# Kernel optimization log

Measured on AMD Instinct MI355X. Metric: run time of the kernel, lower is better.

Reference implementation:

```python
import jax, jax.numpy as jnp
import numpy as np

N = 100000
IN_DIM = 512
OUT_DIM = 512


def setup_inputs() -> dict:
    key = jax.random.key(0)
    k1, k2, k3, k4 = jax.random.split(key, 4)
    x = jax.random.normal(k1, (N, IN_DIM), dtype=jnp.float32)
    edge_index = jax.random.randint(k2, (2, N), 0, N, dtype=jnp.int64)
    # Linear params (torch nn.Linear: out = x @ W.T + b)
    bound = 1.0 / np.sqrt(IN_DIM)
    W = jax.random.uniform(k3, (OUT_DIM, IN_DIM), minval=-bound, maxval=bound, dtype=jnp.float32)
    b = jax.random.uniform(k4, (OUT_DIM,), minval=-bound, maxval=bound, dtype=jnp.float32)
    return {"x": x, "edge_index": edge_index, "W": W, "b": b}


def reference(x, edge_index, W, b):
    # out = relu(linear(x))
    out = jax.nn.relu(jnp.einsum('ni,oi->no', x, W) + b)  # [N, OUT_DIM]
    # torch.scatter_add(out, 0, col[:, None], x):
    # index has shape [E, 1] so only column 0 of src (= x) is scattered:
    # out[col[e], 0] += x[e, 0]
    col = edge_index[1].astype(jnp.int32)  # [E], E == N here
    E = col.shape[0]
    out = out.at[col, 0].add(x[:E, 0])
    return out
```

## Files before the change

kernel.cpp:

```cpp
#include <hip/hip_runtime.h>
#include <stdint.h>

#define K_DIM 512
#define N_OUT 512
#define BM 128
#define BN 128
#define BK 64

typedef __bf16 bf16x8 __attribute__((ext_vector_type(8)));
typedef float f32x4 __attribute__((ext_vector_type(4)));
typedef unsigned short ushort8 __attribute__((ext_vector_type(8)));

__device__ inline unsigned short f2bf(float f) {
  unsigned u = __float_as_uint(f);
  u += 0x7fffu + ((u >> 16) & 1u);
  return (unsigned short)(u >> 16);
}

__global__ __launch_bounds__(256) void cvt_bf16_kernel(const float* __restrict__ src,
                                                       unsigned short* __restrict__ dst,
                                                       int n8) {
  int i = blockIdx.x * 256 + threadIdx.x;
  if (i >= n8) return;
  const float4* s = (const float4*)src + (size_t)i * 2;
  float4 a = s[0], c = s[1];
  ushort8 o;
  o[0] = f2bf(a.x); o[1] = f2bf(a.y); o[2] = f2bf(a.z); o[3] = f2bf(a.w);
  o[4] = f2bf(c.x); o[5] = f2bf(c.y); o[6] = f2bf(c.z); o[7] = f2bf(c.w);
  *(ushort8*)(dst + (size_t)i * 8) = o;
}

__global__ __launch_bounds__(256) void zero_f32_kernel(float* __restrict__ p, int n) {
  int i = blockIdx.x * 256 + threadIdx.x;
  if (i < n) p[i] = 0.f;
}

__global__ __launch_bounds__(256) void scatter_s_kernel(const float* __restrict__ x,
                                                        const int* __restrict__ ei,
                                                        float* __restrict__ s, int E) {
  int e = blockIdx.x * 256 + threadIdx.x;
  if (e < E) {
    int c = ei[E + e];
    atomicAdd(s + c, x[(size_t)e * K_DIM]);
  }
}

__global__ __launch_bounds__(256) void gemm_fused2_kernel(
    const float* __restrict__ x, const unsigned short* __restrict__ wb,
    const float* __restrict__ b, const float* __restrict__ s,
    float* __restrict__ out, int M) {
  __shared__ __align__(16) unsigned short Als[BM * BK];
  __shared__ __align__(16) unsigned short Bls[BN * BK];

  const int tid = threadIdx.x;
  const int lane = tid & 63;
  const int quad = lane >> 4;
  const int l16 = lane & 15;
  const int waveId = tid >> 6;
  const int wm = (waveId >> 1) * 64;
  const int wn = (waveId & 1) * 64;

  const int nwg = gridDim.x * gridDim.y;
  int raw = blockIdx.y * gridDim.x + blockIdx.x;
  int q = nwg >> 3, r = nwg & 7;
  int xcd = raw & 7;
  int wg = (xcd < r ? xcd * (q + 1) : r * (q + 1) + (xcd - r) * q) + (raw >> 3);
  const int blockM = (wg >> 2) * BM;
  const int blockN = (wg & 3) * BN;

  size_t goffA[4], goffB[4];
  int ldsoff[4];
#pragma unroll
  for (int i = 0; i < 4; ++i) {
    int ch = i * 256 + tid;
    int row = ch >> 3;
    int c8 = ch & 7;
    int sc = c8 ^ (row & 7);
    int ga_row = blockM + row;
    if (ga_row > M - 1) ga_row = M - 1;
    goffA[i] = (size_t)ga_row * K_DIM + sc * 8;
    goffB[i] = (size_t)(blockN + row) * K_DIM + sc * 8;
    ldsoff[i] = ch * 8;
  }

  f32x4 acc[4][4] = {};

  for (int k0 = 0; k0 < K_DIM; k0 += BK) {
    float4 a0[4], a1[4];
#pragma unroll
    for (int i = 0; i < 4; ++i) {
      a0[i] = *(const float4*)(x + goffA[i] + k0);
      a1[i] = *(const float4*)(x + goffA[i] + k0 + 4);
    }
#pragma unroll
    for (int i = 0; i < 4; ++i) {
      __builtin_amdgcn_global_load_lds(
          (const __attribute__((address_space(1))) void*)(wb + goffB[i] + k0),
          (__attribute__((address_space(3))) void*)(&Bls[ldsoff[i]]), 16, 0, 0);
    }
#pragma unroll
    for (int i = 0; i < 4; ++i) {
      ushort8 o;
      o[0] = f2bf(a0[i].x); o[1] = f2bf(a0[i].y); o[2] = f2bf(a0[i].z); o[3] = f2bf(a0[i].w);
      o[4] = f2bf(a1[i].x); o[5] = f2bf(a1[i].y); o[6] = f2bf(a1[i].z); o[7] = f2bf(a1[i].w);
      *(ushort8*)(&Als[ldsoff[i]]) = o;
    }
    __syncthreads();

#pragma unroll
    for (int ss = 0; ss < 2; ++ss) {
      bf16x8 af[4], bfr[4];
#pragma unroll
      for (int mi = 0; mi < 4; ++mi) {
        int rr = wm + mi * 16 + l16;
        int c = (ss * 4 + quad) ^ (rr & 7);
        af[mi] = *(const bf16x8*)(&Als[rr * BK + c * 8]);
      }
#pragma unroll
      for (int ni = 0; ni < 4; ++ni) {
        int rr = wn + ni * 16 + l16;
        int c = (ss * 4 + quad) ^ (rr & 7);
        bfr[ni] = *(const bf16x8*)(&Bls[rr * BK + c * 8]);
      }
#pragma unroll
      for (int mi = 0; mi < 4; ++mi)
#pragma unroll
        for (int ni = 0; ni < 4; ++ni)
          acc[mi][ni] = __builtin_amdgcn_mfma_f32_16x16x32_bf16(af[mi], bfr[ni], acc[mi][ni], 0, 0, 0);
    }
    __syncthreads();
  }

#pragma unroll
  for (int ni = 0; ni < 4; ++ni) {
    int gcol = blockN + wn + ni * 16 + l16;
    float bias = b[gcol];
#pragma unroll
    for (int mi = 0; mi < 4; ++mi) {
#pragma unroll
      for (int rr = 0; rr < 4; ++rr) {
        int grow = blockM + wm + mi * 16 + quad * 4 + rr;
        if (grow < M) {
          float v = acc[mi][ni][rr] + bias;
          v = v > 0.f ? v : 0.f;
          if (gcol == 0) v += s[grow];
          __builtin_nontemporal_store(v, out + (size_t)grow * N_OUT + gcol);
        }
      }
    }
  }
}

#define LDS_STRIDE 40
__global__ __launch_bounds__(256) void gemm_fused_kernel(
    const float* __restrict__ x, const float* __restrict__ W,
    const float* __restrict__ b, float* __restrict__ out, int M) {
  __shared__ __align__(16) unsigned short Als[BM * LDS_STRIDE];
  __shared__ __align__(16) unsigned short Bls[BN * LDS_STRIDE];
  const int tid = threadIdx.x;
  const int lane = tid & 63;
  const int quad = lane >> 4;
  const int l16 = lane & 15;
  const int waveId = tid >> 6;
  const int wm = (waveId >> 1) * 64;
  const int wn = (waveId & 1) * 64;
  const int blockM = blockIdx.y * BM;
  const int blockN = blockIdx.x * BN;
  f32x4 acc[4][4] = {};
  for (int k0 = 0; k0 < K_DIM; k0 += 32) {
#pragma unroll
    for (int i = 0; i < 4; ++i) {
      int idx = i * 256 + tid;
      int row = idx >> 3;
      int c4 = idx & 7;
      float4 va = make_float4(0.f, 0.f, 0.f, 0.f);
      int grow = blockM + row;
      if (grow < M) va = *(const float4*)(x + (size_t)grow * K_DIM + k0 + c4 * 4);
      ushort4 ha;
      ha.x = f2bf(va.x); ha.y = f2bf(va.y); ha.z = f2bf(va.z); ha.w = f2bf(va.w);
      *(ushort4*)(&Als[row * LDS_STRIDE + c4 * 4]) = ha;
      float4 vb = *(const float4*)(W + (size_t)(blockN + row) * K_DIM + k0 + c4 * 4);
      ushort4 hb;
      hb.x = f2bf(vb.x); hb.y = f2bf(vb.y); hb.z = f2bf(vb.z); hb.w = f2bf(vb.w);
      *(ushort4*)(&Bls[row * LDS_STRIDE + c4 * 4]) = hb;
    }
    __syncthreads();
    bf16x8 af[4], bfr[4];
#pragma unroll
    for (int mi = 0; mi < 4; ++mi)
      af[mi] = *(const bf16x8*)(&Als[(wm + mi * 16 + l16) * LDS_STRIDE + quad * 8]);
#pragma unroll
    for (int ni = 0; ni < 4; ++ni)
      bfr[ni] = *(const bf16x8*)(&Bls[(wn + ni * 16 + l16) * LDS_STRIDE + quad * 8]);
#pragma unroll
    for (int mi = 0; mi < 4; ++mi)
#pragma unroll
      for (int ni = 0; ni < 4; ++ni)
        acc[mi][ni] = __builtin_amdgcn_mfma_f32_16x16x32_bf16(af[mi], bfr[ni], acc[mi][ni], 0, 0, 0);
    __syncthreads();
  }
#pragma unroll
  for (int ni = 0; ni < 4; ++ni) {
    int gcol = blockN + wn + ni * 16 + l16;
    float bias = b[gcol];
#pragma unroll
    for (int mi = 0; mi < 4; ++mi) {
#pragma unroll
      for (int rr = 0; rr < 4; ++rr) {
        int grow = blockM + wm + mi * 16 + quad * 4 + rr;
        if (grow < M) {
          float v = acc[mi][ni][rr] + bias;
          out[(size_t)grow * N_OUT + gcol] = v > 0.f ? v : 0.f;
        }
      }
    }
  }
}

__global__ void scatter_kernel(const float* __restrict__ x,
                               const int* __restrict__ ei,
                               float* __restrict__ out, int E) {
  int e = blockIdx.x * 256 + threadIdx.x;
  if (e < E) {
    int c = ei[E + e];
    atomicAdd(out + (size_t)c * N_OUT, x[(size_t)e * K_DIM]);
  }
}

extern "C" void kernel_launch(void* const* d_in, const int* in_sizes, int n_in,
                              void* d_out, int out_size, void* d_ws, size_t ws_size,
                              hipStream_t stream) {
  const float* x = (const float*)d_in[0];
  const int* ei = (const int*)d_in[1];
  const float* W = (const float*)d_in[2];
  const float* b = (const float*)d_in[3];
  float* out = (float*)d_out;

  int M = in_sizes[0] / K_DIM;
  int E = in_sizes[1] / 2;

  size_t w_elems = (size_t)N_OUT * K_DIM;
  size_t need = w_elems * 2 + (size_t)M * 4 + 64;

  dim3 grid(N_OUT / BN, (M + BM - 1) / BM);

  if (ws_size >= need) {
    unsigned short* wb = (unsigned short*)d_ws;
    float* s = (float*)((char*)d_ws + w_elems * 2);
    int n8w = (int)(w_elems / 8);
    zero_f32_kernel<<<(M + 255) / 256, 256, 0, stream>>>(s, M);
    scatter_s_kernel<<<(E + 255) / 256, 256, 0, stream>>>(x, ei, s, E);
    cvt_bf16_kernel<<<(n8w + 255) / 256, 256, 0, stream>>>(W, wb, n8w);
    gemm_fused2_kernel<<<grid, 256, 0, stream>>>(x, wb, b, s, out, M);
  } else {
    gemm_fused_kernel<<<grid, 256, 0, stream>>>(x, W, b, out, M);
    scatter_kernel<<<(E + 255) / 256, 256, 0, stream>>>(x, ei, out, E);
  }
}
```

Measured before the change: 478.8 us.

## Double-buffer LDS tiles in GEMM and merge zero/convert prep kernels

The GEMM main loop now uses two LDS buffers for A and B. The next K-tile is prefetched from global memory (x loads into registers, W bf16 via global_load_lds) while MFMAs run on the current tile, which removes one barrier per iteration. The separate zero-fill and W-to-bf16 conversion kernels are merged into one prep kernel to save a launch. LDS use doubles to 64KB per block, which may lower occupancy, and holding prefetched x in registers raises register pressure.

```diff
diff --git a/kernel.cpp b/kernel.cpp
--- a/kernel.cpp
+++ b/kernel.cpp
@@ -17,22 +17,22 @@
   return (unsigned short)(u >> 16);
 }
 
-__global__ __launch_bounds__(256) void cvt_bf16_kernel(const float* __restrict__ src,
-                                                       unsigned short* __restrict__ dst,
-                                                       int n8) {
+__global__ __launch_bounds__(256) void prep_kernel(const float* __restrict__ W,
+                                                   unsigned short* __restrict__ wb,
+                                                   float* __restrict__ s,
+                                                   int n8w, int M) {
   int i = blockIdx.x * 256 + threadIdx.x;
-  if (i >= n8) return;
-  const float4* s = (const float4*)src + (size_t)i * 2;
-  float4 a = s[0], c = s[1];
-  ushort8 o;
-  o[0] = f2bf(a.x); o[1] = f2bf(a.y); o[2] = f2bf(a.z); o[3] = f2bf(a.w);
-  o[4] = f2bf(c.x); o[5] = f2bf(c.y); o[6] = f2bf(c.z); o[7] = f2bf(c.w);
-  *(ushort8*)(dst + (size_t)i * 8) = o;
-}
-
-__global__ __launch_bounds__(256) void zero_f32_kernel(float* __restrict__ p, int n) {
-  int i = blockIdx.x * 256 + threadIdx.x;
-  if (i < n) p[i] = 0.f;
+  if (i < n8w) {
+    const float4* sp = (const float4*)W + (size_t)i * 2;
+    float4 a = sp[0], c = sp[1];
+    ushort8 o;
+    o[0] = f2bf(a.x); o[1] = f2bf(a.y); o[2] = f2bf(a.z); o[3] = f2bf(a.w);
+    o[4] = f2bf(c.x); o[5] = f2bf(c.y); o[6] = f2bf(c.z); o[7] = f2bf(c.w);
+    *(ushort8*)(wb + (size_t)i * 8) = o;
+  } else {
+    int j = i - n8w;
+    if (j < M) s[j] = 0.f;
+  }
 }
 
 __global__ __launch_bounds__(256) void scatter_s_kernel(const float* __restrict__ x,
@@ -49,8 +49,8 @@
     const float* __restrict__ x, const unsigned short* __restrict__ wb,
     const float* __restrict__ b, const float* __restrict__ s,
     float* __restrict__ out, int M) {
-  __shared__ __align__(16) unsigned short Als[BM * BK];
-  __shared__ __align__(16) unsigned short Bls[BN * BK];
+  __shared__ __align__(16) unsigned short Als[2][BM * BK];
+  __shared__ __align__(16) unsigned short Bls[2][BN * BK];
 
   const int tid = threadIdx.x;
   const int lane = tid & 63;
@@ -84,28 +84,43 @@
   }
 
   f32x4 acc[4][4] = {};
-
+  float4 a0[4], a1[4];
+
+#pragma unroll
+  for (int i = 0; i < 4; ++i) {
+    __builtin_amdgcn_global_load_lds(
+        (const __attribute__((address_space(1))) void*)(wb + goffB[i]),
+        (__attribute__((address_space(3))) void*)(&Bls[0][ldsoff[i]]), 16, 0, 0);
+    a0[i] = *(const float4*)(x + goffA[i]);
+    a1[i] = *(const float4*)(x + goffA[i] + 4);
+  }
+#pragma unroll
+  for (int i = 0; i < 4; ++i) {
+    ushort8 o;
+    o[0] = f2bf(a0[i].x); o[1] = f2bf(a0[i].y); o[2] = f2bf(a0[i].z); o[3] = f2bf(a0[i].w);
+    o[4] = f2bf(a1[i].x); o[5] = f2bf(a1[i].y); o[6] = f2bf(a1[i].z); o[7] = f2bf(a1[i].w);
+    *(ushort8*)(&Als[0][ldsoff[i]]) = o;
+  }
+  __syncthreads();
+
+  int cur = 0;
   for (int k0 = 0; k0 < K_DIM; k0 += BK) {
-    float4 a0[4], a1[4];
-#pragma unroll
-    for (int i = 0; i < 4; ++i) {
-      a0[i] = *(const float4*)(x + goffA[i] + k0);
-      a1[i] = *(const float4*)(x + goffA[i] + k0 + 4);
-    }
-#pragma unroll
-    for (int i = 0; i < 4; ++i) {
-      __builtin_amdgcn_global_load_lds(
-          (const __attribute__((address_space(1))) void*)(wb + goffB[i] + k0),
-          (__attribute__((address_space(3))) void*)(&Bls[ldsoff[i]]), 16, 0, 0);
-    }
-#pragma unroll
-    for (int i = 0; i < 4; ++i) {
-      ushort8 o;
-      o[0] = f2bf(a0[i].x); o[1] = f2bf(a0[i].y); o[2] = f2bf(a0[i].z); o[3] = f2bf(a0[i].w);
-      o[4] = f2bf(a1[i].x); o[5] = f2bf(a1[i].y); o[6] = f2bf(a1[i].z); o[7] = f2bf(a1[i].w);
-      *(ushort8*)(&Als[ldsoff[i]]) = o;
-    }
-    __syncthreads();
+    const int nxt = cur ^ 1;
+    const bool has_next = (k0 + BK) < K_DIM;
+
+    if (has_next) {
+#pragma unroll
+      for (int i = 0; i < 4; ++i) {
+        __builtin_amdgcn_global_load_lds(
+            (const __attribute__((address_space(1))) void*)(wb + goffB[i] + k0 + BK),
+            (__attribute__((address_space(3))) void*)(&Bls[nxt][ldsoff[i]]), 16, 0, 0);
+      }
+#pragma unroll
+      for (int i = 0; i < 4; ++i) {
+        a0[i] = *(const float4*)(x + goffA[i] + k0 + BK);
+        a1[i] = *(const float4*)(x + goffA[i] + k0 + BK + 4);
+      }
+    }
 
 #pragma unroll
     for (int ss = 0; ss < 2; ++ss) {
@@ -114,13 +129,13 @@
       for (int mi = 0; mi < 4; ++mi) {
         int rr = wm + mi * 16 + l16;
         int c = (ss * 4 + quad) ^ (rr & 7);
-        af[mi] = *(const bf16x8*)(&Als[rr * BK + c * 8]);
+        af[mi] = *(const bf16x8*)(&Als[cur][rr * BK + c * 8]);
       }
 #pragma unroll
       for (int ni = 0; ni < 4; ++ni) {
         int rr = wn + ni * 16 + l16;
         int c = (ss * 4 + quad) ^ (rr & 7);
-        bfr[ni] = *(const bf16x8*)(&Bls[rr * BK + c * 8]);
+        bfr[ni] = *(const bf16x8*)(&Bls[cur][rr * BK + c * 8]);
       }
 #pragma unroll
       for (int mi = 0; mi < 4; ++mi)
@@ -128,7 +143,19 @@
         for (int ni = 0; ni < 4; ++ni)
           acc[mi][ni] = __builtin_amdgcn_mfma_f32_16x16x32_bf16(af[mi], bfr[ni], acc[mi][ni], 0, 0, 0);
     }
+
+    if (has_next) {
+#pragma unroll
+      for (int i = 0; i < 4; ++i) {
+        ushort8 o;
+        o[0] = f2bf(a0[i].x); o[1] = f2bf(a0[i].y); o[2] = f2bf(a0[i].z); o[3] = f2bf(a0[i].w);
+        o[4] = f2bf(a1[i].x); o[5] = f2bf(a1[i].y); o[6] = f2bf(a1[i].z); o[7] = f2bf(a1[i].w);
+        *(ushort8*)(&Als[nxt][ldsoff[i]]) = o;
+      }
+    }
+
     __syncthreads();
+    cur = nxt;
   }
 
 #pragma unroll
@@ -248,9 +275,9 @@
     unsigned short* wb = (unsigned short*)d_ws;
     float* s = (float*)((char*)d_ws + w_elems * 2);
     int n8w = (int)(w_elems / 8);
-    zero_f32_kernel<<<(M + 255) / 256, 256, 0, stream>>>(s, M);
+    int prep_total = n8w + M;
+    prep_kernel<<<(prep_total + 255) / 256, 256, 0, stream>>>(W, wb, s, n8w, M);
     scatter_s_kernel<<<(E + 255) / 256, 256, 0, stream>>>(x, ei, s, E);
-    cvt_bf16_kernel<<<(n8w + 255) / 256, 256, 0, stream>>>(W, wb, n8w);
     gemm_fused2_kernel<<<grid, 256, 0, stream>>>(x, wb, b, s, out, M);
   } else {
     gemm_fused_kernel<<<grid, 256, 0, stream>>>(x, W, b, out, M);
```

New measurement: 476.0 us. Within noise of the previous version (-0.6%).

## Pre-convert x to bf16 in a fused prep kernel and stream via LDS DMA

Applied to the files above, without the earlier changes.

Adds a single grid-stride prep kernel that converts x and W to bf16, extracts x's first column, and zeroes the scatter buffer, replacing three small kernels. The GEMM then loads both A and B tiles directly into LDS with global_load_lds instead of loading fp32 x and converting in registers. This aims to cut GEMM-side fp32 traffic and conversion ALU work, and to reduce launch count. In exchange it adds a full extra pass writing and re-reading a bf16 copy of x and a larger workspace requirement.

```diff
diff --git a/kernel.cpp b/kernel.cpp
--- a/kernel.cpp
+++ b/kernel.cpp
@@ -17,36 +17,51 @@
   return (unsigned short)(u >> 16);
 }
 
-__global__ __launch_bounds__(256) void cvt_bf16_kernel(const float* __restrict__ src,
-                                                       unsigned short* __restrict__ dst,
-                                                       int n8) {
-  int i = blockIdx.x * 256 + threadIdx.x;
-  if (i >= n8) return;
-  const float4* s = (const float4*)src + (size_t)i * 2;
-  float4 a = s[0], c = s[1];
-  ushort8 o;
-  o[0] = f2bf(a.x); o[1] = f2bf(a.y); o[2] = f2bf(a.z); o[3] = f2bf(a.w);
-  o[4] = f2bf(c.x); o[5] = f2bf(c.y); o[6] = f2bf(c.z); o[7] = f2bf(c.w);
-  *(ushort8*)(dst + (size_t)i * 8) = o;
-}
-
-__global__ __launch_bounds__(256) void zero_f32_kernel(float* __restrict__ p, int n) {
-  int i = blockIdx.x * 256 + threadIdx.x;
-  if (i < n) p[i] = 0.f;
-}
-
-__global__ __launch_bounds__(256) void scatter_s_kernel(const float* __restrict__ x,
+__global__ __launch_bounds__(256) void prep_all_kernel(
+    const float* __restrict__ x, unsigned short* __restrict__ xb,
+    const float* __restrict__ W, unsigned short* __restrict__ wb,
+    float* __restrict__ x0, float* __restrict__ s,
+    int n8x, int n8w, int n8s) {
+  const int stride = gridDim.x * 256;
+  const int total = n8x + n8w + n8s;
+  for (int i = blockIdx.x * 256 + threadIdx.x; i < total; i += stride) {
+    if (i < n8x) {
+      const f32x4* sp = (const f32x4*)x + (size_t)i * 2;
+      f32x4 a = __builtin_nontemporal_load(sp);
+      f32x4 c = __builtin_nontemporal_load(sp + 1);
+      ushort8 o;
+      o[0] = f2bf(a[0]); o[1] = f2bf(a[1]); o[2] = f2bf(a[2]); o[3] = f2bf(a[3]);
+      o[4] = f2bf(c[0]); o[5] = f2bf(c[1]); o[6] = f2bf(c[2]); o[7] = f2bf(c[3]);
+      *(ushort8*)(xb + (size_t)i * 8) = o;
+      if ((i & 63) == 0) x0[i >> 6] = a[0];
+    } else if (i < n8x + n8w) {
+      int j = i - n8x;
+      const f32x4* sp = (const f32x4*)W + (size_t)j * 2;
+      f32x4 a = sp[0], c = sp[1];
+      ushort8 o;
+      o[0] = f2bf(a[0]); o[1] = f2bf(a[1]); o[2] = f2bf(a[2]); o[3] = f2bf(a[3]);
+      o[4] = f2bf(c[0]); o[5] = f2bf(c[1]); o[6] = f2bf(c[2]); o[7] = f2bf(c[3]);
+      *(ushort8*)(wb + (size_t)j * 8) = o;
+    } else {
+      int j = i - n8x - n8w;
+      f32x4 z = {0.f, 0.f, 0.f, 0.f};
+      *(f32x4*)(s + (size_t)j * 8) = z;
+      *(f32x4*)(s + (size_t)j * 8 + 4) = z;
+    }
+  }
+}
+
+__global__ __launch_bounds__(256) void scatter_s_kernel(const float* __restrict__ x0,
                                                         const int* __restrict__ ei,
                                                         float* __restrict__ s, int E) {
   int e = blockIdx.x * 256 + threadIdx.x;
   if (e < E) {
-    int c = ei[E + e];
-    atomicAdd(s + c, x[(size_t)e * K_DIM]);
-  }
-}
-
-__global__ __launch_bounds__(256) void gemm_fused2_kernel(
-    const float* __restrict__ x, const unsigned short* __restrict__ wb,
+    atomicAdd(s + ei[E + e], x0[e]);
+  }
+}
+
+__global__ __launch_bounds__(256) void gemm_bf16_kernel(
+    const unsigned short* __restrict__ xb, const unsigned short* __restrict__ wb,
     const float* __restrict__ b, const float* __restrict__ s,
     float* __restrict__ out, int M) {
   __shared__ __align__(16) unsigned short Als[BM * BK];
@@ -86,24 +101,14 @@
   f32x4 acc[4][4] = {};
 
   for (int k0 = 0; k0 < K_DIM; k0 += BK) {
-    float4 a0[4], a1[4];
 #pragma unroll
     for (int i = 0; i < 4; ++i) {
-      a0[i] = *(const float4*)(x + goffA[i] + k0);
-      a1[i] = *(const float4*)(x + goffA[i] + k0 + 4);
-    }
-#pragma unroll
-    for (int i = 0; i < 4; ++i) {
+      __builtin_amdgcn_global_load_lds(
+          (const __attribute__((address_space(1))) void*)(xb + goffA[i] + k0),
+          (__attribute__((address_space(3))) void*)(&Als[ldsoff[i]]), 16, 0, 0);
       __builtin_amdgcn_global_load_lds(
           (const __attribute__((address_space(1))) void*)(wb + goffB[i] + k0),
           (__attribute__((address_space(3))) void*)(&Bls[ldsoff[i]]), 16, 0, 0);
-    }
-#pragma unroll
-    for (int i = 0; i < 4; ++i) {
-      ushort8 o;
-      o[0] = f2bf(a0[i].x); o[1] = f2bf(a0[i].y); o[2] = f2bf(a0[i].z); o[3] = f2bf(a0[i].w);
-      o[4] = f2bf(a1[i].x); o[5] = f2bf(a1[i].y); o[6] = f2bf(a1[i].z); o[7] = f2bf(a1[i].w);
-      *(ushort8*)(&Als[ldsoff[i]]) = o;
     }
     __syncthreads();
 
@@ -239,19 +244,29 @@
   int M = in_sizes[0] / K_DIM;
   int E = in_sizes[1] / 2;
 
+  size_t x_elems = (size_t)M * K_DIM;
   size_t w_elems = (size_t)N_OUT * K_DIM;
-  size_t need = w_elems * 2 + (size_t)M * 4 + 64;
+  int n8x = (int)(x_elems / 8);
+  int n8w = (int)(w_elems / 8);
+  int n8s = (M + 7) / 8;
+  size_t s_elems = (size_t)n8s * 8;
+
+  size_t need = x_elems * 2 + w_elems * 2 + s_elems * 4 + (size_t)M * 4;
 
   dim3 grid(N_OUT / BN, (M + BM - 1) / BM);
 
   if (ws_size >= need) {
-    unsigned short* wb = (unsigned short*)d_ws;
-    float* s = (float*)((char*)d_ws + w_elems * 2);
-    int n8w = (int)(w_elems / 8);
-    zero_f32_kernel<<<(M + 255) / 256, 256, 0, stream>>>(s, M);
-    scatter_s_kernel<<<(E + 255) / 256, 256, 0, stream>>>(x, ei, s, E);
-    cvt_bf16_kernel<<<(n8w + 255) / 256, 256, 0, stream>>>(W, wb, n8w);
-    gemm_fused2_kernel<<<grid, 256, 0, stream>>>(x, wb, b, s, out, M);
+    unsigned short* xb = (unsigned short*)d_ws;
+    unsigned short* wb = xb + x_elems;
+    float* s = (float*)(wb + w_elems);
+    float* x0 = s + s_elems;
+
+    int total = n8x + n8w + n8s;
+    int pblk = (total + 255) / 256;
+    if (pblk > 2048) pblk = 2048;
+    prep_all_kernel<<<pblk, 256, 0, stream>>>(x, xb, W, wb, x0, s, n8x, n8w, n8s);
+    scatter_s_kernel<<<(E + 255) / 256, 256, 0, stream>>>(x0, ei, s, E);
+    gemm_bf16_kernel<<<grid, 256, 0, stream>>>(xb, wb, b, s, out, M);
   } else {
     gemm_fused_kernel<<<grid, 256, 0, stream>>>(x, W, b, out, M);
     scatter_kernel<<<(E + 255) / 256, 256, 0, stream>>>(x, ei, out, E);
```

New measurement: 452.9 us. 1.06x faster.
